# Kernel tuning notes

Measured on AMD Instinct MI355X. Metric: run time of the kernel, lower is better.

Reference implementation:

```python
import jax, jax.numpy as jnp
import numpy as np

B, N, QN, C, H = 4, 1024, 512, 1024, 16
D = C // H  # head_dim = 64


def setup_inputs() -> dict:
    key = jax.random.key(0)
    ks = jax.random.split(key, 8)
    w = lambda k, shape: jax.random.normal(k, shape, jnp.float32) * 0.02
    return dict(
        x=jax.random.normal(ks[0], (B, N, C), jnp.float32),
        query=jax.random.normal(ks[1], (B, QN, C), jnp.float32),
        w_qkv=w(ks[2], (3 * C, C)),        # self.qkv (no bias)
        w_kv=w(ks[3], (2 * C, C)),         # self.to_query_kv (no bias)
        w_qlin=w(ks[4], (3 * C, C)),       # self.query_linear (no bias)
        gate=jnp.zeros((1, H, 1, 1), jnp.float32),  # zero-initialized gate param
        w_proj=w(ks[5], (C, C)),
        b_proj=jnp.zeros((C,), jnp.float32),
        w_qproj=w(ks[6], (C, C)),
        b_qproj=jnp.zeros((C,), jnp.float32),
    )


def _sdpa(q, k, v, scale):
    # q,k,v: [B,H,S,D]; standard softmax attention (attn_mask=None, p=0)
    s = jnp.einsum('bhqd,bhkd->bhqk', q, k) * scale
    return jnp.einsum('bhqk,bhkd->bhqd', jax.nn.softmax(s, axis=-1), v)


def reference(x, query, w_qkv, w_kv, w_qlin, gate, w_proj, b_proj, w_qproj, b_qproj):
    scale = 1.0 / np.sqrt(D)
    # qkv on x -> [3,B,H,N,D]
    qkv = (x @ w_qkv.T).reshape(B, N, 3, H, D).transpose(2, 0, 3, 1, 4)
    q, k, v = qkv[0], qkv[1], qkv[2]
    # kv for cross path computed from ORIGINAL x (before self-attn), as in torch code
    kv = (x @ w_kv.T).reshape(B, N, 2, H, D).transpose(2, 0, 3, 1, 4)
    xk0, xv0 = kv[0], kv[1]
    # self-attention on x (x_mask=None)
    x_attn = _sdpa(q, k, v, scale)  # [B,H,N,D]
    # query qkv -> [3,B,H,QN,D]
    qq3 = (query @ w_qlin.T).reshape(B, QN, 3, H, D).transpose(2, 0, 3, 1, 4)
    qq, qk, qv = qq3[0], qq3[1], qq3[2]
    xk = jnp.concatenate([xk0, qk], axis=2)  # [B,H,N+QN,D]
    xv = jnp.concatenate([xv0, qv], axis=2)
    scores = jnp.einsum('bhqd,bhkd->bhqk', qq, xk) * scale  # [B,H,QN,N+QN]
    # split softmax with tanh-gated first segment (mask=None; dropout p=0)
    gated = jnp.concatenate(
        [jnp.tanh(gate) * jax.nn.softmax(scores[..., :N], axis=-1),
         jax.nn.softmax(scores[..., N:], axis=-1)], axis=-1)
    q_attn = jnp.einsum('bhqk,bhkd->bhqd', gated, xv)  # [B,H,QN,D]
    x_out = x_attn.transpose(0, 2, 1, 3).reshape(B, N, C) @ w_proj.T + b_proj
    q_out = q_attn.transpose(0, 2, 1, 3).reshape(B, QN, C) @ w_qproj.T + b_qproj
    return (x_out, q_out)
```

## Files before the change

### kernel.cpp

```cpp
#include <hip/hip_runtime.h>


using bf16 = __bf16;
typedef __bf16 bf16x4 __attribute__((ext_vector_type(4)));
typedef __bf16 bf16x8 __attribute__((ext_vector_type(8)));
typedef float  f32x4  __attribute__((ext_vector_type(4)));
typedef float  f32x16 __attribute__((ext_vector_type(16)));
typedef unsigned int u32x4 __attribute__((ext_vector_type(4)));

#define MFMA16(a, b, c) __builtin_amdgcn_mfma_f32_16x16x32_bf16((a), (b), (c), 0, 0, 0)
#define MFMA32(a, b, c) __builtin_amdgcn_mfma_f32_32x32x16_bf16((a), (b), (c), 0, 0, 0)

__device__ __forceinline__ int swz128(int row) { return ((row ^ (row >> 3)) & 7) << 4; }

__device__ __forceinline__ void gl_lds16(const void* g, void* l) {
  __builtin_amdgcn_global_load_lds(
      (const __attribute__((address_space(1))) unsigned int*)g,
      (__attribute__((address_space(3))) unsigned int*)l, 16, 0, 0);
}

__device__ __forceinline__ unsigned pack2(float a, float b) {
  unsigned short ua = __builtin_bit_cast(unsigned short, (bf16)a);
  unsigned short ub = __builtin_bit_cast(unsigned short, (bf16)b);
  return (unsigned)ua | ((unsigned)ub << 16);
}

__device__ __forceinline__ float exp2_fast(float x) {
  float r;
  asm("v_exp_f32 %0, %1" : "=v"(r) : "v"(x));
  return r;
}

__global__ void k_cast_all(const float* __restrict__ s0, const float* __restrict__ s1,
                           const float* __restrict__ s2, const float* __restrict__ s3,
                           const float* __restrict__ s4, const float* __restrict__ s5,
                           const float* __restrict__ s6, bf16* __restrict__ dst) {
  constexpr size_t MM = 1u << 20;
  constexpr size_t o1 = 4 * MM, o2 = 6 * MM, o3 = 9 * MM, o4 = 11 * MM,
                   o5 = 14 * MM, o6 = 15 * MM, total = 16 * MM;
  size_t stride = (size_t)gridDim.x * blockDim.x * 8;
  for (size_t i = ((size_t)blockIdx.x * blockDim.x + threadIdx.x) * 8; i < total; i += stride) {
    const float* s; size_t loc;
    if (i < o1)      { s = s0; loc = i; }
    else if (i < o2) { s = s1; loc = i - o1; }
    else if (i < o3) { s = s2; loc = i - o2; }
    else if (i < o4) { s = s3; loc = i - o3; }
    else if (i < o5) { s = s4; loc = i - o4; }
    else if (i < o6) { s = s5; loc = i - o5; }
    else             { s = s6; loc = i - o6; }
    float4 a = *(const float4*)(s + loc);
    float4 b = *(const float4*)(s + loc + 4);
    bf16x8 o;
    o[0] = (bf16)a.x; o[1] = (bf16)a.y; o[2] = (bf16)a.z; o[3] = (bf16)a.w;
    o[4] = (bf16)b.x; o[5] = (bf16)b.y; o[6] = (bf16)b.z; o[7] = (bf16)b.w;
    *(bf16x8*)(dst + i) = o;
  }
}

template<int MODE, int N>
__global__ __launch_bounds__(256)
void k_gemm(const bf16* __restrict__ A, const bf16* __restrict__ B0,
            const bf16* __restrict__ B1,
            const float* __restrict__ bias0, const float* __restrict__ bias1,
            bf16* __restrict__ RM, bf16* __restrict__ VTa, bf16* __restrict__ VTb,
            float* __restrict__ OUT) {
  constexpr int K = 1024;
  __shared__ bf16 As[128 * 64];
  __shared__ bf16 Bs[128 * 64];
  const int tid = threadIdx.x;
  const int lane = tid & 63, w = tid >> 6;
  const int wr = w >> 1, wc = w & 1;
  const int nbx = N / 128;
  const int bid = ((int)blockIdx.x & 7) * ((int)gridDim.x >> 3) + ((int)blockIdx.x >> 3);
  const int tm = (bid / nbx) * 128, tn = (bid % nbx) * 128;
  const int r0 = lane & 15, kg = lane >> 4;
  const bf16* Bp = B0;
  if constexpr (MODE == 0) { if (tm >= 4096) Bp = B1; }
  f32x4 acc[4][4] = {};
  for (int kk = 0; kk < K; kk += 64) {
#pragma unroll
    for (int i = 0; i < 4; i++) {
      int c = i * 256 + tid;
      int row = c >> 3, kb = c & 7;
      int sb = (kb ^ ((row ^ (row >> 3)) & 7)) * 8;
      gl_lds16(A + (size_t)(tm + row) * K + kk + sb, (char*)As + c * 16);
      gl_lds16(Bp + (size_t)(tn + row) * K + kk + sb, (char*)Bs + c * 16);
    }
    __syncthreads();
#pragma unroll
    for (int ks = 0; ks < 2; ks++) {
      bf16x8 af[4], bfv[4];
#pragma unroll
      for (int f = 0; f < 4; f++) {
        int rowa = wr * 64 + f * 16 + r0;
        af[f] = *(const bf16x8*)((const char*)As +
                                 ((rowa * 128 + ks * 64 + kg * 16) ^ swz128(rowa)));
        int rowb = wc * 64 + f * 16 + r0;
        bfv[f] = *(const bf16x8*)((const char*)Bs +
                                  ((rowb * 128 + ks * 64 + kg * 16) ^ swz128(rowb)));
      }
#pragma unroll
      for (int mf = 0; mf < 4; mf++)
#pragma unroll
        for (int nf = 0; nf < 4; nf++)
          acc[mf][nf] = MFMA16(af[mf], bfv[nf], acc[mf][nf]);
    }
    __syncthreads();
  }
#pragma unroll
  for (int mf = 0; mf < 4; mf++) {
    const int rowb = tm + wr * 64 + mf * 16 + kg * 4;
#pragma unroll
    for (int nf = 0; nf < 4; nf++) {
      const int coln = tn + wc * 64 + nf * 16 + r0;
      if constexpr (MODE == 0) {
        const float* bias = (tm < 4096) ? bias0 : bias1;
        float bv = bias[coln & 1023];
#pragma unroll
        for (int j = 0; j < 4; j++)
          OUT[(size_t)(rowb + j) * 1024 + (coln & 1023)] = acc[mf][nf][j] + bv;
      } else {
        bool rm; int rmcol = coln, base = 0, tokb = 10, rs_ = 3072;
        bf16* vt = VTa;
        if constexpr (MODE == 1) {
          if (tn < 2048)      { rm = true; }
          else if (tn < 3072) { rm = false; base = 2048; }
          else if (tn < 4096) { rm = true; rmcol = coln - 1024; }
          else                { rm = false; base = 4096; vt = VTb; }
        } else {
          rs_ = 2048; tokb = 9;
          if (tn < 2048) { rm = true; }
          else           { rm = false; base = 2048; }
        }
        if (rm) {
#pragma unroll
          for (int j = 0; j < 4; j++)
            RM[(size_t)(rowb + j) * rs_ + rmcol] = (bf16)acc[mf][nf][j];
        } else {
          int dg = coln - base, h_ = dg >> 6, dd = dg & 63;
          int bq = rowb >> tokb, tok = rowb & ((1 << tokb) - 1);
          bf16x4 wv;
#pragma unroll
          for (int j = 0; j < 4; j++) wv[j] = (bf16)acc[mf][nf][j];
          *(bf16x4*)(vt + (((size_t)((bq * 16 + h_) * 64 + dd)) << tokb) + tok) = wv;
        }
      }
    }
  }
}

template<int NT>
__device__ __forceinline__ void attn_pass32(
    const bf16* __restrict__ Kg, int kRS,
    const bf16* __restrict__ VTg, int vRS,
    int ntiles, const bf16x8* qf, bf16* Ks, bf16* Vt,
    f32x16* o, float& m, float& rs) {
  const int tid = threadIdx.x;
  const int lane = tid & 63;
  const int lq = lane & 31, kg2 = lane >> 5;

  auto stage = [&](const bf16* base, int rstride, int colofs, bf16* dst) {
#pragma unroll
    for (int i = 0; i < 512 / NT; i++) {
      int c = i * NT + tid;
      int r = c >> 3, kb = c & 7;
      int sb = (kb ^ ((r ^ (r >> 3)) & 7)) * 8;
      gl_lds16(base + (size_t)r * rstride + colofs + sb, (char*)dst + c * 16);
    }
  };

  stage(Kg, kRS, 0, Ks);
  stage(VTg, vRS, 0, Vt);
  __syncthreads();

  for (int t = 0; t < ntiles; t++) {
    bf16* KsC = Ks + (t & 1) * 4096;
    bf16* VtC = Vt + (t & 1) * 4096;
    const bool more = (t + 1 < ntiles);
    if (more) {
      stage(Kg + (size_t)(t + 1) * 64 * kRS, kRS, 0, Ks + ((t & 1) ^ 1) * 4096);
      stage(VTg, vRS, (t + 1) * 64, Vt + ((t & 1) ^ 1) * 4096);
    }

    f32x16 s[2];
    s[0] = (f32x16)0.f; s[1] = (f32x16)0.f;
    __builtin_amdgcn_s_setprio(1);
#pragma unroll
    for (int kb = 0; kb < 2; kb++) {
      int row = kb * 32 + lq;
#pragma unroll
      for (int dw = 0; dw < 4; dw++) {
        bf16x8 kf = *(const bf16x8*)((const char*)KsC +
                                     ((row * 128 + dw * 32 + kg2 * 16) ^ swz128(row)));
        s[kb] = MFMA32(kf, qf[dw], s[kb]);
      }
    }
    __builtin_amdgcn_s_setprio(0);

    float vmax = s[0][0];
#pragma unroll
    for (int j = 1; j < 16; j++) vmax = fmaxf(vmax, s[0][j]);
#pragma unroll
    for (int j = 0; j < 16; j++) vmax = fmaxf(vmax, s[1][j]);
    vmax = fmaxf(vmax, __shfl_xor(vmax, 32, 64));
    if (__any(vmax > m + 11.5f)) {
      float mn = fmaxf(m, vmax);
      float fac = exp2_fast(m - mn);
      m = mn;
      rs *= fac;
#pragma unroll
      for (int j = 0; j < 16; j++) {
        int rowq = (j & 3) + 8 * (j >> 2) + 4 * kg2;
        float fj = __shfl(fac, rowq, 64);
        o[0][j] *= fj;
        o[1][j] *= fj;
      }
    }
    float tsum = 0.f;
    f32x16 p[2];
#pragma unroll
    for (int kb = 0; kb < 2; kb++)
#pragma unroll
      for (int j = 0; j < 16; j++) {
        float pv = exp2_fast(s[kb][j] - m);
        p[kb][j] = pv;
        tsum += pv;
      }
    tsum += __shfl_xor(tsum, 32, 64);
    rs += tsum;

    unsigned pk[2][4][2];
#pragma unroll
    for (int kb = 0; kb < 2; kb++)
#pragma unroll
      for (int n = 0; n < 4; n++) {
        pk[kb][n][0] = pack2(p[kb][4 * n + 0], p[kb][4 * n + 1]);
        pk[kb][n][1] = pack2(p[kb][4 * n + 2], p[kb][4 * n + 3]);
      }

#pragma unroll
    for (int w = 0; w < 4; w++) {
      const int kb = w >> 1, wb = w & 1;
      unsigned pushA = kg2 ? pk[kb][2 * wb][0] : pk[kb][2 * wb + 1][0];
      unsigned pushB = kg2 ? pk[kb][2 * wb][1] : pk[kb][2 * wb + 1][1];
      unsigned rcvA = __shfl_xor(pushA, 32, 64);
      unsigned rcvB = __shfl_xor(pushB, 32, 64);
      u32x4 fu;
      fu[0] = kg2 ? rcvA : pk[kb][2 * wb][0];
      fu[1] = kg2 ? rcvB : pk[kb][2 * wb][1];
      fu[2] = kg2 ? pk[kb][2 * wb + 1][0] : rcvA;
      fu[3] = kg2 ? pk[kb][2 * wb + 1][1] : rcvB;
      bf16x8 pfrag = __builtin_bit_cast(bf16x8, fu);
      __builtin_amdgcn_s_setprio(1);
#pragma unroll
      for (int db = 0; db < 2; db++) {
        int d = db * 32 + lq;
        bf16x8 vf = *(const bf16x8*)((const char*)VtC +
                                     ((d * 128 + w * 32 + kg2 * 16) ^ swz128(d)));
        o[db] = MFMA32(pfrag, vf, o[db]);
      }
      __builtin_amdgcn_s_setprio(0);
    }

    __syncthreads();
  }
}

__global__ __launch_bounds__(256)
void k_attn(const bf16* __restrict__ XK, const bf16* __restrict__ QQK,
            const bf16* __restrict__ VTs, const bf16* __restrict__ VT0,
            const bf16* __restrict__ VTq, const float* __restrict__ gate,
            bf16* __restrict__ xat, bf16* __restrict__ qat) {
  __shared__ bf16 Ks[2 * 4096], Vt[2 * 4096];
  const int pb = blockIdx.x;
  const int bid = (pb & 7) * 96 + (pb >> 3);
  const int bh = bid / 12, r = bid % 12;
  const int b = bh >> 4, h = bh & 15;
  const int tid = threadIdx.x, lane = tid & 63, wv = tid >> 6;
  const int lq = lane & 31, kg2 = lane >> 5;
  constexpr float QS = 0.125f * 1.44269504088896f;

  if (r < 8) {
    const int qtok = b * 1024 + r * 128 + wv * 32;
    bf16x8 qf[4];
#pragma unroll
    for (int dw = 0; dw < 4; dw++) {
      qf[dw] = *(const bf16x8*)(XK + (size_t)(qtok + lq) * 3072 + h * 64 + dw * 16 + kg2 * 8);
#pragma unroll
      for (int e = 0; e < 8; e++) qf[dw][e] = (bf16)((float)qf[dw][e] * QS);
    }
    f32x16 o[2];
    o[0] = (f32x16)0.f; o[1] = (f32x16)0.f;
    float m = -__builtin_inff(), rs = 0.f;
    attn_pass32<256>(XK + (size_t)(b * 1024) * 3072 + 1024 + h * 64, 3072,
                     VTs + (size_t)bh * 64 * 1024, 1024,
                     16, qf, Ks, Vt, o, m, rs);
#pragma unroll
    for (int j = 0; j < 16; j++) {
      int rowq = (j & 3) + 8 * (j >> 2) + 4 * kg2;
      float rsj = __shfl(rs, rowq, 64);
      size_t base = (size_t)(qtok + rowq) * 1024 + h * 64;
      xat[base + lq] = (bf16)(o[0][j] / rsj);
      xat[base + 32 + lq] = (bf16)(o[1][j] / rsj);
    }
  } else {
    const int qt = r - 8;
    const int qtok = b * 512 + qt * 128 + wv * 32;
    bf16x8 qf[4];
#pragma unroll
    for (int dw = 0; dw < 4; dw++) {
      qf[dw] = *(const bf16x8*)(QQK + (size_t)(qtok + lq) * 2048 + h * 64 + dw * 16 + kg2 * 8);
#pragma unroll
      for (int e = 0; e < 8; e++) qf[dw][e] = (bf16)((float)qf[dw][e] * QS);
    }
    const float g = tanhf(gate[h]);
    unsigned pka[2][8] = {};
    f32x16 o[2];
    o[0] = (f32x16)0.f; o[1] = (f32x16)0.f;
    float m, rs;
    if (g != 0.0f) {
      m = -__builtin_inff(); rs = 0.f;
      attn_pass32<256>(XK + (size_t)(b * 1024) * 3072 + 2048 + h * 64, 3072,
                       VT0 + (size_t)bh * 64 * 1024, 1024,
                       16, qf, Ks, Vt, o, m, rs);
#pragma unroll
      for (int j2 = 0; j2 < 8; j2++) {
        int j0 = 2 * j2;
        int rq0 = (j0 & 3) + 8 * (j0 >> 2) + 4 * kg2;
        float ra = __shfl(rs, rq0, 64);
        float rb = __shfl(rs, rq0 + 1, 64);
        pka[0][j2] = pack2(g * o[0][j0] / ra, g * o[0][j0 + 1] / rb);
        pka[1][j2] = pack2(g * o[1][j0] / ra, g * o[1][j0 + 1] / rb);
      }
      o[0] = (f32x16)0.f; o[1] = (f32x16)0.f;
    }
    m = -__builtin_inff(); rs = 0.f;
    attn_pass32<256>(QQK + (size_t)(b * 512) * 2048 + 1024 + h * 64, 2048,
                     VTq + (size_t)bh * 64 * 512, 512,
                     8, qf, Ks, Vt, o, m, rs);
#pragma unroll
    for (int j = 0; j < 16; j++) {
      int rowq = (j & 3) + 8 * (j >> 2) + 4 * kg2;
      float rsj = __shfl(rs, rowq, 64);
      size_t base = (size_t)(qtok + rowq) * 1024 + h * 64;
      unsigned wa = pka[0][j >> 1], wb = pka[1][j >> 1];
      unsigned short ua = (j & 1) ? (unsigned short)(wa >> 16) : (unsigned short)(wa & 0xffffu);
      unsigned short ub = (j & 1) ? (unsigned short)(wb >> 16) : (unsigned short)(wb & 0xffffu);
      float a0 = (float)__builtin_bit_cast(bf16, ua);
      float a1 = (float)__builtin_bit_cast(bf16, ub);
      qat[base + lq] = (bf16)(o[0][j] / rsj + a0);
      qat[base + 32 + lq] = (bf16)(o[1][j] / rsj + a1);
    }
  }
}

extern "C" void kernel_launch(void* const* d_in, const int* in_sizes, int n_in,
                              void* d_out, int out_size, void* d_ws, size_t ws_size,
                              hipStream_t stream) {
  (void)in_sizes; (void)n_in; (void)out_size; (void)ws_size;
  const float* x       = (const float*)d_in[0];
  const float* query   = (const float*)d_in[1];
  const float* w_qkv   = (const float*)d_in[2];
  const float* w_kv    = (const float*)d_in[3];
  const float* w_qlin  = (const float*)d_in[4];
  const float* gate    = (const float*)d_in[5];
  const float* w_proj  = (const float*)d_in[6];
  const float* b_proj  = (const float*)d_in[7];
  const float* w_qproj = (const float*)d_in[8];
  const float* b_qproj = (const float*)d_in[9];
  float* out = (float*)d_out;

  bf16* p = (bf16*)d_ws;
  bf16* xb = p;      p += (size_t)4096 * 1024;
  bf16* qb = p;      p += (size_t)2048 * 1024;
  bf16* wqkvb = p;   p += (size_t)3072 * 1024;
  bf16* wkvb = p;    p += (size_t)2048 * 1024;
  bf16* wqlinb = p;  p += (size_t)3072 * 1024;
  bf16* wprojb = p;  p += (size_t)1024 * 1024;
  bf16* wqprojb = p; p += (size_t)1024 * 1024;
  bf16* XK = p;      p += (size_t)4096 * 3072;
  bf16* VTs = p;     p += (size_t)64 * 64 * 1024;
  bf16* VT0 = p;     p += (size_t)64 * 64 * 1024;
  bf16* QQK = p;     p += (size_t)2048 * 2048;
  bf16* VTq = p;     p += (size_t)64 * 64 * 512;
  bf16* xat = p;     p += (size_t)4096 * 1024;
  bf16* qat = p;     p += (size_t)2048 * 1024;

  k_cast_all<<<2048, 256, 0, stream>>>(x, query, w_qkv, w_kv, w_qlin, w_proj, w_qproj,
                                       (bf16*)d_ws);

  k_gemm<1, 5120><<<dim3(32 * 40), 256, 0, stream>>>(
      xb, wqkvb, nullptr, nullptr, nullptr, XK, VTs, VT0, nullptr);
  k_gemm<2, 3072><<<dim3(16 * 24), 256, 0, stream>>>(
      qb, wqlinb, nullptr, nullptr, nullptr, QQK, VTq, nullptr, nullptr);

  k_attn<<<dim3(768), 256, 0, stream>>>(XK, QQK, VTs, VT0, VTq, gate, xat, qat);

  k_gemm<0, 1024><<<dim3(48 * 8), 256, 0, stream>>>(
      xat, wprojb, wqprojb, b_proj, b_qproj, nullptr, nullptr, nullptr, out);
}
```

Before: 199.9 us.

## Merge QKV GEMMs into one 256x256 triple-buffered kernel; triple-buffer attention K/V

The two input-projection GEMMs become one launch, k_gemm_big, using 256x256 tiles, 512 threads and a three-stage global-to-LDS pipeline with explicit vmcnt waits instead of full syncthreads. The attention inner loop gets the same three-buffer prefetch, staging two tiles ahead. The goal is to hide memory latency, raise data reuse per tile and save one launch. In exchange it uses more LDS and registers per block, which may cut occupancy, and the hand-placed waitcnt counts must match the number of in-flight loads exactly.

New measurement: 193.5 us. -3.2%, faster.

```diff
diff --git a/kernel.cpp b/kernel.cpp
--- a/kernel.cpp
+++ b/kernel.cpp
@@ -30,6 +30,9 @@
   asm("v_exp_f32 %0, %1" : "=v"(r) : "v"(x));
   return r;
 }
+
+#define WAITV(N) asm volatile("s_waitcnt vmcnt(" #N ")" ::: "memory")
+#define RAW_BAR() do { __builtin_amdgcn_s_barrier(); asm volatile("" ::: "memory"); } while (0)
 
 __global__ void k_cast_all(const float* __restrict__ s0, const float* __restrict__ s1,
                            const float* __restrict__ s2, const float* __restrict__ s3,
@@ -57,14 +60,116 @@
   }
 }
 
-template<int MODE, int N>
+__global__ __launch_bounds__(512, 2)
+void k_gemm_big(const bf16* __restrict__ xb, const bf16* __restrict__ qb,
+                const bf16* __restrict__ wqkvb, const bf16* __restrict__ wqlinb,
+                bf16* __restrict__ XK, bf16* __restrict__ VTs, bf16* __restrict__ VT0,
+                bf16* __restrict__ QQK, bf16* __restrict__ VTq) {
+  constexpr int K = 1024, NK = 32;
+  __shared__ bf16 As[3 * 256 * 32];
+  __shared__ bf16 Bs[3 * 256 * 32];
+  const int tid = threadIdx.x;
+  const int lane = tid & 63, w = tid >> 6;
+  const int wm = w >> 2, wn = w & 3;
+  const int r0 = lane & 15, kg = lane >> 4;
+  const int bid = ((int)blockIdx.x & 7) * 52 + ((int)blockIdx.x >> 3);
+  int grp, tm, tn;
+  const bf16 *Ap, *Bp;
+  if (bid < 320) { grp = 0; tm = (bid / 20) * 256; tn = (bid % 20) * 256; Ap = xb; Bp = wqkvb; }
+  else { grp = 1; int t = bid - 320; tm = (t / 12) * 256; tn = (t % 12) * 256; Ap = qb; Bp = wqlinb; }
+
+  auto stage = [&](int step, int bi) {
+    const int kk = step * 32;
+#pragma unroll
+    for (int j = 0; j < 2; j++) {
+      int c = j * 512 + tid;
+      int row = c >> 2, kb = c & 3;
+      int sg = (kb ^ ((row >> 1) & 3)) * 8;
+      gl_lds16(Ap + (size_t)(tm + row) * K + kk + sg, (char*)As + bi * 16384 + c * 16);
+    }
+#pragma unroll
+    for (int j = 0; j < 2; j++) {
+      int c = j * 512 + tid;
+      int row = c >> 2, kb = c & 3;
+      int sg = (kb ^ ((row >> 1) & 3)) * 8;
+      gl_lds16(Bp + (size_t)(tn + row) * K + kk + sg, (char*)Bs + bi * 16384 + c * 16);
+    }
+  };
+
+  f32x4 acc[8][4] = {};
+  stage(0, 0);
+  stage(1, 1);
+  WAITV(4);
+  RAW_BAR();
+
+  for (int t = 0; t < NK; t++) {
+    const int bi = t % 3;
+    const bool more = (t + 2 < NK);
+    if (more) stage(t + 2, (t + 2) % 3);
+    const char* Ab = (const char*)As + bi * 16384;
+    const char* Bb = (const char*)Bs + bi * 16384;
+    bf16x8 af[8], bfv[4];
+#pragma unroll
+    for (int mf = 0; mf < 8; mf++) {
+      int row = wm * 128 + mf * 16 + r0;
+      af[mf] = *(const bf16x8*)(Ab + row * 64 + ((kg ^ ((row >> 1) & 3)) << 4));
+    }
+#pragma unroll
+    for (int nf = 0; nf < 4; nf++) {
+      int row = wn * 64 + nf * 16 + r0;
+      bfv[nf] = *(const bf16x8*)(Bb + row * 64 + ((kg ^ ((row >> 1) & 3)) << 4));
+    }
+    __builtin_amdgcn_s_setprio(1);
+#pragma unroll
+    for (int mf = 0; mf < 8; mf++)
+#pragma unroll
+      for (int nf = 0; nf < 4; nf++)
+        acc[mf][nf] = MFMA16(af[mf], bfv[nf], acc[mf][nf]);
+    __builtin_amdgcn_s_setprio(0);
+    if (more) { WAITV(4); } else { WAITV(0); }
+    RAW_BAR();
+  }
+
+#pragma unroll
+  for (int mf = 0; mf < 8; mf++) {
+    const int rowb = tm + wm * 128 + mf * 16 + kg * 4;
+#pragma unroll
+    for (int nf = 0; nf < 4; nf++) {
+      const int coln = tn + wn * 64 + nf * 16 + r0;
+      bool rm; int rmcol = coln, vbase = 0, tokb = 10, rs_ = 3072;
+      bf16* vt = VTs;
+      bf16* rmp = XK;
+      if (grp == 0) {
+        if (tn < 2048)      { rm = true; }
+        else if (tn < 3072) { rm = false; vbase = 2048; vt = VTs; }
+        else if (tn < 4096) { rm = true; rmcol = coln - 1024; }
+        else                { rm = false; vbase = 4096; vt = VT0; }
+      } else {
+        rs_ = 2048; tokb = 9; rmp = QQK;
+        if (tn < 2048) { rm = true; }
+        else           { rm = false; vbase = 2048; vt = VTq; }
+      }
+      if (rm) {
+#pragma unroll
+        for (int j = 0; j < 4; j++)
+          rmp[(size_t)(rowb + j) * rs_ + rmcol] = (bf16)acc[mf][nf][j];
+      } else {
+        int dg = coln - vbase, h_ = dg >> 6, dd = dg & 63;
+        int bq = rowb >> tokb, tok = rowb & ((1 << tokb) - 1);
+        bf16x4 wv;
+#pragma unroll
+        for (int j = 0; j < 4; j++) wv[j] = (bf16)acc[mf][nf][j];
+        *(bf16x4*)(vt + (((size_t)((bq * 16 + h_) * 64 + dd)) << tokb) + tok) = wv;
+      }
+    }
+  }
+}
+
 __global__ __launch_bounds__(256)
-void k_gemm(const bf16* __restrict__ A, const bf16* __restrict__ B0,
-            const bf16* __restrict__ B1,
-            const float* __restrict__ bias0, const float* __restrict__ bias1,
-            bf16* __restrict__ RM, bf16* __restrict__ VTa, bf16* __restrict__ VTb,
-            float* __restrict__ OUT) {
-  constexpr int K = 1024;
+void k_gemm_proj(const bf16* __restrict__ A, const bf16* __restrict__ B0,
+                 const bf16* __restrict__ B1, const float* __restrict__ bias0,
+                 const float* __restrict__ bias1, float* __restrict__ OUT) {
+  constexpr int K = 1024, N = 1024;
   __shared__ bf16 As[128 * 64];
   __shared__ bf16 Bs[128 * 64];
   const int tid = threadIdx.x;
@@ -74,8 +179,8 @@
   const int bid = ((int)blockIdx.x & 7) * ((int)gridDim.x >> 3) + ((int)blockIdx.x >> 3);
   const int tm = (bid / nbx) * 128, tn = (bid % nbx) * 128;
   const int r0 = lane & 15, kg = lane >> 4;
-  const bf16* Bp = B0;
-  if constexpr (MODE == 0) { if (tm >= 4096) Bp = B1; }
+  const bf16* Bp = (tm < 4096) ? B0 : B1;
+  const float* bias = (tm < 4096) ? bias0 : bias1;
   f32x4 acc[4][4] = {};
   for (int kk = 0; kk < K; kk += 64) {
 #pragma unroll
@@ -108,45 +213,16 @@
     __syncthreads();
   }
 #pragma unroll
-  for (int mf = 0; mf < 4; mf++) {
-    const int rowb = tm + wr * 64 + mf * 16 + kg * 4;
-#pragma unroll
-    for (int nf = 0; nf < 4; nf++) {
-      const int coln = tn + wc * 64 + nf * 16 + r0;
-      if constexpr (MODE == 0) {
-        const float* bias = (tm < 4096) ? bias0 : bias1;
-        float bv = bias[coln & 1023];
-#pragma unroll
-        for (int j = 0; j < 4; j++)
-          OUT[(size_t)(rowb + j) * 1024 + (coln & 1023)] = acc[mf][nf][j] + bv;
-      } else {
-        bool rm; int rmcol = coln, base = 0, tokb = 10, rs_ = 3072;
-        bf16* vt = VTa;
-        if constexpr (MODE == 1) {
-          if (tn < 2048)      { rm = true; }
-          else if (tn < 3072) { rm = false; base = 2048; }
-          else if (tn < 4096) { rm = true; rmcol = coln - 1024; }
-          else                { rm = false; base = 4096; vt = VTb; }
-        } else {
-          rs_ = 2048; tokb = 9;
-          if (tn < 2048) { rm = true; }
-          else           { rm = false; base = 2048; }
-        }
-        if (rm) {
-#pragma unroll
-          for (int j = 0; j < 4; j++)
-            RM[(size_t)(rowb + j) * rs_ + rmcol] = (bf16)acc[mf][nf][j];
-        } else {
-          int dg = coln - base, h_ = dg >> 6, dd = dg & 63;
-          int bq = rowb >> tokb, tok = rowb & ((1 << tokb) - 1);
-          bf16x4 wv;
-#pragma unroll
-          for (int j = 0; j < 4; j++) wv[j] = (bf16)acc[mf][nf][j];
-          *(bf16x4*)(vt + (((size_t)((bq * 16 + h_) * 64 + dd)) << tokb) + tok) = wv;
-        }
-      }
-    }
-  }
+  for (int mf = 0; mf < 4; mf++)
+#pragma unroll
+    for (int j = 0; j < 4; j++) {
+      int row = tm + wr * 64 + mf * 16 + kg * 4 + j;
+#pragma unroll
+      for (int nf = 0; nf < 4; nf++) {
+        int col = tn + wc * 64 + nf * 16 + r0;
+        OUT[(size_t)row * 1024 + col] = acc[mf][nf][j] + bias[col];
+      }
+    }
 }
 
 template<int NT>
@@ -159,28 +235,36 @@
   const int lane = tid & 63;
   const int lq = lane & 31, kg2 = lane >> 5;
 
-  auto stage = [&](const bf16* base, int rstride, int colofs, bf16* dst) {
+  auto stage = [&](int t) {
+    bf16* kd = Ks + (t % 3) * 4096;
+    bf16* vd = Vt + (t % 3) * 4096;
+    const bf16* kt = Kg + (size_t)t * 64 * kRS;
 #pragma unroll
     for (int i = 0; i < 512 / NT; i++) {
       int c = i * NT + tid;
       int r = c >> 3, kb = c & 7;
       int sb = (kb ^ ((r ^ (r >> 3)) & 7)) * 8;
-      gl_lds16(base + (size_t)r * rstride + colofs + sb, (char*)dst + c * 16);
+      gl_lds16(kt + (size_t)r * kRS + sb, (char*)kd + c * 16);
+    }
+#pragma unroll
+    for (int i = 0; i < 512 / NT; i++) {
+      int c = i * NT + tid;
+      int r = c >> 3, kb = c & 7;
+      int sb = (kb ^ ((r ^ (r >> 3)) & 7)) * 8;
+      gl_lds16(VTg + (size_t)r * vRS + t * 64 + sb, (char*)vd + c * 16);
     }
   };
 
-  stage(Kg, kRS, 0, Ks);
-  stage(VTg, vRS, 0, Vt);
-  __syncthreads();
+  stage(0);
+  stage(1);
+  WAITV(4);
+  RAW_BAR();
 
   for (int t = 0; t < ntiles; t++) {
-    bf16* KsC = Ks + (t & 1) * 4096;
-    bf16* VtC = Vt + (t & 1) * 4096;
-    const bool more = (t + 1 < ntiles);
-    if (more) {
-      stage(Kg + (size_t)(t + 1) * 64 * kRS, kRS, 0, Ks + ((t & 1) ^ 1) * 4096);
-      stage(VTg, vRS, (t + 1) * 64, Vt + ((t & 1) ^ 1) * 4096);
-    }
+    const char* KsC = (const char*)(Ks + (t % 3) * 4096);
+    const char* VtC = (const char*)(Vt + (t % 3) * 4096);
+    const bool more = (t + 2 < ntiles);
+    if (more) stage(t + 2);
 
     f32x16 s[2];
     s[0] = (f32x16)0.f; s[1] = (f32x16)0.f;
@@ -190,8 +274,7 @@
       int row = kb * 32 + lq;
 #pragma unroll
       for (int dw = 0; dw < 4; dw++) {
-        bf16x8 kf = *(const bf16x8*)((const char*)KsC +
-                                     ((row * 128 + dw * 32 + kg2 * 16) ^ swz128(row)));
+        bf16x8 kf = *(const bf16x8*)(KsC + ((row * 128 + dw * 32 + kg2 * 16) ^ swz128(row)));
         s[kb] = MFMA32(kf, qf[dw], s[kb]);
       }
     }
@@ -255,14 +338,14 @@
 #pragma unroll
       for (int db = 0; db < 2; db++) {
         int d = db * 32 + lq;
-        bf16x8 vf = *(const bf16x8*)((const char*)VtC +
-                                     ((d * 128 + w * 32 + kg2 * 16) ^ swz128(d)));
+        bf16x8 vf = *(const bf16x8*)(VtC + ((d * 128 + w * 32 + kg2 * 16) ^ swz128(d)));
         o[db] = MFMA32(pfrag, vf, o[db]);
       }
       __builtin_amdgcn_s_setprio(0);
     }
 
-    __syncthreads();
+    if (more) { WAITV(4); } else { WAITV(0); }
+    RAW_BAR();
   }
 }
 
@@ -271,7 +354,7 @@
             const bf16* __restrict__ VTs, const bf16* __restrict__ VT0,
             const bf16* __restrict__ VTq, const float* __restrict__ gate,
             bf16* __restrict__ xat, bf16* __restrict__ qat) {
-  __shared__ bf16 Ks[2 * 4096], Vt[2 * 4096];
+  __shared__ bf16 Ks[3 * 4096], Vt[3 * 4096];
   const int pb = blockIdx.x;
   const int bid = (pb & 7) * 96 + (pb >> 3);
   const int bh = bid / 12, r = bid % 12;
@@ -385,17 +468,15 @@
   bf16* VTq = p;     p += (size_t)64 * 64 * 512;
   bf16* xat = p;     p += (size_t)4096 * 1024;
   bf16* qat = p;     p += (size_t)2048 * 1024;
+  (void)wkvb;
 
   k_cast_all<<<2048, 256, 0, stream>>>(x, query, w_qkv, w_kv, w_qlin, w_proj, w_qproj,
                                        (bf16*)d_ws);
 
-  k_gemm<1, 5120><<<dim3(32 * 40), 256, 0, stream>>>(
-      xb, wqkvb, nullptr, nullptr, nullptr, XK, VTs, VT0, nullptr);
-  k_gemm<2, 3072><<<dim3(16 * 24), 256, 0, stream>>>(
-      qb, wqlinb, nullptr, nullptr, nullptr, QQK, VTq, nullptr, nullptr);
+  k_gemm_big<<<dim3(416), 512, 0, stream>>>(xb, qb, wqkvb, wqlinb,
+                                            XK, VTs, VT0, QQK, VTq);
 
   k_attn<<<dim3(768), 256, 0, stream>>>(XK, QQK, VTs, VT0, VTq, gate, xat, qat);
 
-  k_gemm<0, 1024><<<dim3(48 * 8), 256, 0, stream>>>(
-      xat, wprojb, wqprojb, b_proj, b_qproj, nullptr, nullptr, nullptr, out);
-}
+  k_gemm_proj<<<dim3(48 * 8), 256, 0, stream>>>(xat, wprojb, wqprojb, b_proj, b_qproj, out);
+}
```
